# Optimization experiments

Hardware: AMD Instinct MI355X
Metric: run time of the kernel (lower is better)

Reference implementation:

```python
import jax, jax.numpy as jnp
import numpy as np

N_NODES = 100000
N_EDGES = 1600000
D_IN = 128
HID = 128
N_CLS = 10
N_GRAPHS = 128


def _gcn_conv(x, W, b, src, dst, dis, n):
    # x' = W x; out[i] = sum_{(j->i)} d_j^{-1/2} d_i^{-1/2} x'_j ; then + bias
    h = x @ W  # [N, out]
    norm = dis[src] * dis[dst]  # [E_tot]
    msg = h[src] * norm[:, None]  # gather + scale (irregular access)
    out = jax.ops.segment_sum(msg, dst, num_segments=n)  # scatter-add
    return out + b


def setup_inputs() -> dict:
    key = jax.random.key(0)
    ks = jax.random.split(key, 12)
    x = jax.random.normal(ks[0], (N_NODES, D_IN), dtype=jnp.float32)
    edge_index = jax.random.randint(ks[1], (2, N_EDGES), 0, N_NODES, dtype=jnp.int64)
    batch = jnp.sort(jax.random.randint(ks[2], (N_NODES,), 0, N_GRAPHS, dtype=jnp.int64))
    drop_u = jax.random.uniform(ks[3], (N_NODES, D_IN), dtype=jnp.float32)
    s = lambda k, sh, fan: jax.random.normal(k, sh, dtype=jnp.float32) / np.sqrt(fan)
    return {
        "x": x, "edge_index": edge_index, "batch": batch, "num_graphs": N_GRAPHS,
        "drop_u": drop_u,
        "lin1_w": s(ks[4], (D_IN, D_IN), D_IN), "lin1_b": jnp.zeros((D_IN,), jnp.float32),
        "conv1_w": s(ks[5], (D_IN, HID), D_IN), "conv1_b": jnp.zeros((HID,), jnp.float32),
        "conv2_w": s(ks[6], (HID, HID // 2), HID), "conv2_b": jnp.zeros((HID // 2,), jnp.float32),
        "lin2_w": s(ks[7], (HID // 2, N_CLS), HID // 2), "lin2_b": jnp.zeros((N_CLS,), jnp.float32),
    }


def reference(x, edge_index, batch, num_graphs, drop_u,
              lin1_w, lin1_b, conv1_w, conv1_b, conv2_w, conv2_b, lin2_w, lin2_b):
    n = x.shape[0]
    # add self loops (PyG GCNConv default)
    loop = jnp.arange(n, dtype=edge_index.dtype)
    src = jnp.concatenate([edge_index[0], loop])
    dst = jnp.concatenate([edge_index[1], loop])
    deg = jax.ops.segment_sum(jnp.ones_like(dst, dtype=x.dtype), dst, num_segments=n)
    dis = jnp.where(deg > 0, jax.lax.rsqrt(deg), 0.0)  # deg^{-1/2}

    h = x @ lin1_w + lin1_b
    h = _gcn_conv(h, conv1_w, conv1_b, src, dst, dis, n)
    # dropout p=0.5 (training mode in original): keep where u >= 0.5, scale by 2
    h = h * (drop_u >= 0.5).astype(h.dtype) * 2.0
    h = jax.nn.relu(h)
    h = _gcn_conv(h, conv2_w, conv2_b, src, dst, dis, n)
    # global mean pool over graph ids
    sums = jax.ops.segment_sum(h, batch, num_segments=num_graphs)
    cnts = jax.ops.segment_sum(jnp.ones((n,), h.dtype), batch, num_segments=num_graphs)
    pooled = sums / jnp.maximum(cnts, 1.0)[:, None]
    return pooled @ lin2_w + lin2_b
```

## Files before the change

kernel.cpp:

```cpp
#include <hip/hip_runtime.h>
#include <hip/hip_bf16.h>

#define DIN   128
#define HID2  64
#define NCLS  10
#define NGRAPH 128
#define SCAN_CHUNK 1024
#define NBLK 256
#define NBKT_MAX 512
#define CAP 6144

typedef __attribute__((ext_vector_type(8))) short bf16x8;
typedef __attribute__((ext_vector_type(4))) float f32x4;

__device__ __forceinline__ void atomAddF(float* p, float v) {
    unsafeAtomicAdd(p, v);
}

__device__ __forceinline__ unsigned short f2bf(float f) {
    unsigned int u = __float_as_uint(f);
    u += 0x7fffu + ((u >> 16) & 1u);
    return (unsigned short)(u >> 16);
}

__global__ __launch_bounds__(128) void k_w12(const float* __restrict__ lw,
                                             const float* __restrict__ lb,
                                             const float* __restrict__ cw,
                                             const float* __restrict__ cw2,
                                             float* __restrict__ W12,
                                             float* __restrict__ c1preb,
                                             unsigned short* __restrict__ w2b) {
    int i = blockIdx.x, j = threadIdx.x;
    if (i == 129) {
        for (int f = j; f < 8192; f += 128) w2b[f] = f2bf(cw2[f]);
        return;
    }
    const float* arow = (i < 128) ? (lw + i * 128) : lb;
    float acc = 0.f;
#pragma unroll 8
    for (int k = 0; k < 128; ++k) acc += arow[k] * cw[k * 128 + j];
    if (i < 128) W12[i * 128 + j] = acc;
    else         c1preb[j] = acc;
}

__global__ __launch_bounds__(256) void k_bhist(const int* __restrict__ dst,
                                               int* __restrict__ bh, int E, int nbkt,
                                               float* __restrict__ zbuf, int zn) {
    __shared__ int lh[NBKT_MAX];
    if (blockIdx.x == 0)
        for (int i = threadIdx.x; i < zn; i += 256) zbuf[i] = 0.f;
    for (int i = threadIdx.x; i < nbkt; i += 256) lh[i] = 0;
    __syncthreads();
    for (int e = blockIdx.x * 256 + threadIdx.x; e < E; e += NBLK * 256)
        atomicAdd(&lh[__builtin_nontemporal_load(dst + e) >> 8], 1);
    __syncthreads();
    for (int i = threadIdx.x; i < nbkt; i += 256) bh[i * NBLK + blockIdx.x] = lh[i];
}

__global__ __launch_bounds__(256) void k_scan_part(const int* __restrict__ cnt,
                                                   int* __restrict__ part, int n) {
    int base = blockIdx.x * SCAN_CHUNK + threadIdx.x * 4;
    int s = 0;
#pragma unroll
    for (int j = 0; j < 4; ++j) { int i = base + j; if (i < n) s += cnt[i]; }
#pragma unroll
    for (int o = 32; o > 0; o >>= 1) s += __shfl_down(s, o);
    __shared__ int wsum[4];
    if ((threadIdx.x & 63) == 0) wsum[threadIdx.x >> 6] = s;
    __syncthreads();
    if (threadIdx.x == 0) part[blockIdx.x] = wsum[0] + wsum[1] + wsum[2] + wsum[3];
}
__global__ __launch_bounds__(256) void k_scan_mid(int* __restrict__ part,
                                                  int* __restrict__ total_out,
                                                  int B, int n) {
    __shared__ int sh[256];
    int t = threadIdx.x;
    int v = (t < B) ? part[t] : 0;
    sh[t] = v;
    __syncthreads();
    for (int off = 1; off < 256; off <<= 1) {
        int u = (t >= off) ? sh[t - off] : 0;
        __syncthreads();
        sh[t] += u;
        __syncthreads();
    }
    if (t < B) part[t] = sh[t] - v;
    if (t == 255) total_out[n] = sh[255];
}
__global__ __launch_bounds__(256) void k_scan_fin2(const int* cnt,
                                                   const int* __restrict__ part,
                                                   int* out, int n) {
    __shared__ int sh[256];
    int t = threadIdx.x;
    int base = blockIdx.x * SCAN_CHUNK + t * 4;
    int c[4]; int s = 0;
#pragma unroll
    for (int j = 0; j < 4; ++j) { int i = base + j; c[j] = (i < n) ? cnt[i] : 0; s += c[j]; }
    sh[t] = s;
    __syncthreads();
    for (int off = 1; off < 256; off <<= 1) {
        int u = (t >= off) ? sh[t - off] : 0;
        __syncthreads();
        sh[t] += u;
        __syncthreads();
    }
    int excl = part[blockIdx.x] + sh[t] - s;
#pragma unroll
    for (int j = 0; j < 4; ++j) {
        int i = base + j;
        if (i < n) out[i] = excl;
        excl += c[j];
    }
}

__global__ __launch_bounds__(256) void k_partition(const int* __restrict__ src,
                                                   const int* __restrict__ dst,
                                                   const int* __restrict__ bh,
                                                   int* __restrict__ pairs, int E, int nbkt) {
    __shared__ int cur[NBKT_MAX];
    for (int i = threadIdx.x; i < nbkt; i += 256) cur[i] = bh[i * NBLK + blockIdx.x];
    __syncthreads();
    for (int e = blockIdx.x * 256 + threadIdx.x; e < E; e += NBLK * 256) {
        int d = __builtin_nontemporal_load(dst + e);
        int s = __builtin_nontemporal_load(src + e);
        int pos = atomicAdd(&cur[d >> 8], 1);
        pairs[pos] = (s << 8) | (d & 255);
    }
}

__global__ __launch_bounds__(256) void k_csr_local(const int* __restrict__ pairs,
                                                   const int* __restrict__ bh,
                                                   int* __restrict__ row_start,
                                                   float* __restrict__ dis,
                                                   int* __restrict__ col,
                                                   int N) {
    __shared__ int cntL[256], scanL[256], curL[256];
    __shared__ int srcbuf[CAP];
    const int tid = threadIdx.x;
    const int lo = blockIdx.x << 8;
    const int bstart = bh[blockIdx.x * NBLK];
    const int bend = bh[(blockIdx.x + 1) * NBLK];
    const int nE = bend - bstart;

    cntL[tid] = 0;
    __syncthreads();
    for (int e = bstart + tid; e < bend; e += 256)
        atomicAdd(&cntL[pairs[e] & 255], 1);
    __syncthreads();
    const int deg = cntL[tid];
    scanL[tid] = deg;
    __syncthreads();
    for (int off = 1; off < 256; off <<= 1) {
        int u = (tid >= off) ? scanL[tid - off] : 0;
        __syncthreads();
        scanL[tid] += u;
        __syncthreads();
    }
    const int excl = scanL[tid] - deg;
    curL[tid] = excl;
    const int node = lo + tid;
    if (node < N) {
        row_start[node] = bstart + excl;
        dis[node] = rsqrtf((float)(deg + 1));
    } else if (node == N) {
        row_start[N] = bend;
    }
    __syncthreads();
    if (nE <= CAP) {
        for (int e = bstart + tid; e < bend; e += 256) {
            int p = pairs[e];
            int pos = atomicAdd(&curL[p & 255], 1);
            srcbuf[pos] = ((unsigned int)p) >> 8;
        }
        __syncthreads();
        for (int i = tid; i < nE; i += 256)
            col[bstart + i] = srcbuf[i];
    } else {
        for (int e = bstart + tid; e < bend; e += 256) {
            int p = pairs[e];
            int pos = atomicAdd(&curL[p & 255], 1);
            col[bstart + pos] = ((unsigned int)p) >> 8;
        }
    }
}

template <int NCOL>
__global__ __launch_bounds__(256) void k_gemm_mfma(const float* __restrict__ A,
                                                   const float* __restrict__ W,
                                                   const float* __restrict__ bias,
                                                   unsigned short* __restrict__ out, int M) {
    constexpr int KP = 136;
    __shared__ unsigned short As[64 * KP];
    __shared__ unsigned short Wt[NCOL * KP];

    const int tid = threadIdx.x;
    const int row0 = blockIdx.x * 64;

    for (int f = tid; f < 2048; f += 256) {
        int r = f >> 5, c4 = f & 31;
        int gr = row0 + r;
        float4 v = make_float4(0.f, 0.f, 0.f, 0.f);
        if (gr < M) v = *(const float4*)(A + (size_t)gr * 128 + c4 * 4);
        ushort4 b;
        b.x = f2bf(v.x); b.y = f2bf(v.y); b.z = f2bf(v.z); b.w = f2bf(v.w);
        *(ushort4*)(&As[r * KP + c4 * 4]) = b;
    }
    for (int f = tid; f < 32 * NCOL; f += 256) {
        int k = f / (NCOL / 4), n4 = f % (NCOL / 4);
        float4 v = *(const float4*)(W + (size_t)k * NCOL + n4 * 4);
        Wt[(n4 * 4 + 0) * KP + k] = f2bf(v.x);
        Wt[(n4 * 4 + 1) * KP + k] = f2bf(v.y);
        Wt[(n4 * 4 + 2) * KP + k] = f2bf(v.z);
        Wt[(n4 * 4 + 3) * KP + k] = f2bf(v.w);
    }
    __syncthreads();

    const int wave = tid >> 6, lane = tid & 63;
    const int quad = lane >> 4, l16 = lane & 15;
    constexpr int CT = (NCOL == 128) ? 2 : 1;
    const int col0 = wave * 16 * CT;

    f32x4 acc[4][CT];
#pragma unroll
    for (int rt = 0; rt < 4; ++rt)
#pragma unroll
        for (int ct = 0; ct < CT; ++ct) acc[rt][ct] = 0.f;

#pragma unroll
    for (int ks = 0; ks < 4; ++ks) {
        const int kbase = ks * 32 + quad * 8;
        bf16x8 bfr[CT];
#pragma unroll
        for (int ct = 0; ct < CT; ++ct)
            bfr[ct] = *(const bf16x8*)(&Wt[(col0 + ct * 16 + l16) * KP + kbase]);
#pragma unroll
        for (int rt = 0; rt < 4; ++rt) {
            bf16x8 afr = *(const bf16x8*)(&As[(rt * 16 + l16) * KP + kbase]);
#pragma unroll
            for (int ct = 0; ct < CT; ++ct)
                acc[rt][ct] = __builtin_amdgcn_mfma_f32_16x16x32_bf16(afr, bfr[ct], acc[rt][ct], 0, 0, 0);
        }
    }

#pragma unroll
    for (int rt = 0; rt < 4; ++rt)
#pragma unroll
        for (int ct = 0; ct < CT; ++ct) {
            const int c = col0 + ct * 16 + l16;
            const float bv = bias ? bias[c] : 0.f;
#pragma unroll
            for (int reg = 0; reg < 4; ++reg) {
                const int gr = row0 + rt * 16 + quad * 4 + reg;
                if (gr < M) out[(size_t)gr * NCOL + c] = f2bf(acc[rt][ct][reg] + bv);
            }
        }
}

__device__ __forceinline__ void bfacc(uint4 v, float d, float* acc) {
    acc[0] = fmaf(d, __uint_as_float(v.x << 16),        acc[0]);
    acc[1] = fmaf(d, __uint_as_float(v.x & 0xffff0000u), acc[1]);
    acc[2] = fmaf(d, __uint_as_float(v.y << 16),        acc[2]);
    acc[3] = fmaf(d, __uint_as_float(v.y & 0xffff0000u), acc[3]);
    acc[4] = fmaf(d, __uint_as_float(v.z << 16),        acc[4]);
    acc[5] = fmaf(d, __uint_as_float(v.z & 0xffff0000u), acc[5]);
    acc[6] = fmaf(d, __uint_as_float(v.w << 16),        acc[6]);
    acc[7] = fmaf(d, __uint_as_float(v.w & 0xffff0000u), acc[7]);
}

__global__ __launch_bounds__(256) void k_gather_gemm2(const unsigned short* __restrict__ h,
                                                      const int* __restrict__ row_start,
                                                      const int* __restrict__ col,
                                                      const float* __restrict__ dis,
                                                      const float* __restrict__ bias,
                                                      const float* __restrict__ du,
                                                      const unsigned short* __restrict__ w2b,
                                                      unsigned short* __restrict__ h2b,
                                                      int n) {
    constexpr int KP = 136;
    __shared__ unsigned short As[16 * KP];
    __shared__ unsigned short Wt[64 * KP];
    const int tid = threadIdx.x;
    const int node0 = blockIdx.x * 16;
    const int node = node0 + (tid >> 4);
    const int l = tid & 15;
    const int coff = l * 8;

    for (int f = tid; f < 8192; f += 256) {
        int k = f >> 6, c = f & 63;
        Wt[c * KP + k] = w2b[f];
    }

    float r[8];
    if (node < n) {
        const float dn = dis[node];
        float acc[8];
        {
            uint4 v = *(const uint4*)(h + (size_t)node * 128 + coff);
#pragma unroll
            for (int q = 0; q < 8; ++q) acc[q] = 0.f;
            bfacc(v, dn, acc);
        }
        const int beg = row_start[node], end = row_start[node + 1];
        int j = beg;
        for (; j + 3 < end; j += 4) {
            const int s0 = col[j], s1 = col[j + 1], s2 = col[j + 2], s3 = col[j + 3];
            const float d0 = dis[s0], d1 = dis[s1], d2 = dis[s2], d3 = dis[s3];
            const uint4 v0 = *(const uint4*)(h + (size_t)s0 * 128 + coff);
            const uint4 v1 = *(const uint4*)(h + (size_t)s1 * 128 + coff);
            const uint4 v2 = *(const uint4*)(h + (size_t)s2 * 128 + coff);
            const uint4 v3 = *(const uint4*)(h + (size_t)s3 * 128 + coff);
            bfacc(v0, d0, acc);
            bfacc(v1, d1, acc);
            bfacc(v2, d2, acc);
            bfacc(v3, d3, acc);
        }
        for (; j < end; ++j) {
            const int s0 = col[j];
            const float d0 = dis[s0];
            const uint4 v0 = *(const uint4*)(h + (size_t)s0 * 128 + coff);
            bfacc(v0, d0, acc);
        }
        const float4 b0 = *(const float4*)(bias + coff);
        const float4 b1 = *(const float4*)(bias + coff + 4);
        r[0] = fmaf(dn, acc[0], b0.x); r[1] = fmaf(dn, acc[1], b0.y);
        r[2] = fmaf(dn, acc[2], b0.z); r[3] = fmaf(dn, acc[3], b0.w);
        r[4] = fmaf(dn, acc[4], b1.x); r[5] = fmaf(dn, acc[5], b1.y);
        r[6] = fmaf(dn, acc[6], b1.z); r[7] = fmaf(dn, acc[7], b1.w);
        const float4 u0 = *(const float4*)(du + (size_t)node * 128 + coff);
        const float4 u1 = *(const float4*)(du + (size_t)node * 128 + coff + 4);
        r[0] = (u0.x >= 0.5f) ? 2.f * fmaxf(r[0], 0.f) : 0.f;
        r[1] = (u0.y >= 0.5f) ? 2.f * fmaxf(r[1], 0.f) : 0.f;
        r[2] = (u0.z >= 0.5f) ? 2.f * fmaxf(r[2], 0.f) : 0.f;
        r[3] = (u0.w >= 0.5f) ? 2.f * fmaxf(r[3], 0.f) : 0.f;
        r[4] = (u1.x >= 0.5f) ? 2.f * fmaxf(r[4], 0.f) : 0.f;
        r[5] = (u1.y >= 0.5f) ? 2.f * fmaxf(r[5], 0.f) : 0.f;
        r[6] = (u1.z >= 0.5f) ? 2.f * fmaxf(r[6], 0.f) : 0.f;
        r[7] = (u1.w >= 0.5f) ? 2.f * fmaxf(r[7], 0.f) : 0.f;
    } else {
#pragma unroll
        for (int q = 0; q < 8; ++q) r[q] = 0.f;
    }
    ushort4 o0, o1;
    o0.x = f2bf(r[0]); o0.y = f2bf(r[1]); o0.z = f2bf(r[2]); o0.w = f2bf(r[3]);
    o1.x = f2bf(r[4]); o1.y = f2bf(r[5]); o1.z = f2bf(r[6]); o1.w = f2bf(r[7]);
    *(ushort4*)(&As[(tid >> 4) * KP + coff]) = o0;
    *(ushort4*)(&As[(tid >> 4) * KP + coff + 4]) = o1;
    __syncthreads();

    const int wave = tid >> 6, lane = tid & 63;
    const int quad = lane >> 4, l16 = lane & 15;
    const int c0 = wave * 16;
    f32x4 a2 = 0.f;
#pragma unroll
    for (int ks = 0; ks < 4; ++ks) {
        const int kbase = ks * 32 + quad * 8;
        bf16x8 afr = *(const bf16x8*)(&As[l16 * KP + kbase]);
        bf16x8 bfr = *(const bf16x8*)(&Wt[(c0 + l16) * KP + kbase]);
        a2 = __builtin_amdgcn_mfma_f32_16x16x32_bf16(afr, bfr, a2, 0, 0, 0);
    }
#pragma unroll
    for (int reg = 0; reg < 4; ++reg) {
        const int gr = node0 + quad * 4 + reg;
        if (gr < n) h2b[(size_t)gr * 64 + c0 + l16] = f2bf(a2[reg]);
    }
}

__global__ __launch_bounds__(256) void k_gather_pool(const unsigned short* __restrict__ h,
                                                     const int* __restrict__ row_start,
                                                     const int* __restrict__ col,
                                                     const float* __restrict__ dis,
                                                     const float* __restrict__ bias,
                                                     const int* __restrict__ batch,
                                                     float* __restrict__ partial,
                                                     int* __restrict__ bgid,
                                                     int* __restrict__ bvcnt,
                                                     float* __restrict__ sums,
                                                     float* __restrict__ cnt, int n) {
    __shared__ float bsum[4][64];
    __shared__ int sh_gfirst, sh_uni;
    const int tid = threadIdx.x;
    const int node = (blockIdx.x * 256 + tid) >> 3;
    const int l = tid & 7;
    const int coff = l * 8;
    const bool valid = node < n;
    const int node0 = blockIdx.x * 32;

    if (tid == 0) { sh_gfirst = batch[node0]; sh_uni = 1; }
    __syncthreads();
    const int gfirst = sh_gfirst;

    float r[8];
    int g = gfirst;
    if (valid) {
        const float dn = dis[node];
        g = batch[node];
        float acc[8];
        {
            uint4 v = *(const uint4*)(h + (size_t)node * 64 + coff);
#pragma unroll
            for (int q = 0; q < 8; ++q) acc[q] = 0.f;
            bfacc(v, dn, acc);
        }
        const int beg = row_start[node], end = row_start[node + 1];
        int j = beg;
        for (; j + 3 < end; j += 4) {
            const int s0 = col[j], s1 = col[j + 1], s2 = col[j + 2], s3 = col[j + 3];
            const float d0 = dis[s0], d1 = dis[s1], d2 = dis[s2], d3 = dis[s3];
            const uint4 v0 = *(const uint4*)(h + (size_t)s0 * 64 + coff);
            const uint4 v1 = *(const uint4*)(h + (size_t)s1 * 64 + coff);
            const uint4 v2 = *(const uint4*)(h + (size_t)s2 * 64 + coff);
            const uint4 v3 = *(const uint4*)(h + (size_t)s3 * 64 + coff);
            bfacc(v0, d0, acc);
            bfacc(v1, d1, acc);
            bfacc(v2, d2, acc);
            bfacc(v3, d3, acc);
        }
        for (; j < end; ++j) {
            const int s0 = col[j];
            const float d0 = dis[s0];
            const uint4 v0 = *(const uint4*)(h + (size_t)s0 * 64 + coff);
            bfacc(v0, d0, acc);
        }
        const float4 b0 = *(const float4*)(bias + coff);
        const float4 b1 = *(const float4*)(bias + coff + 4);
        r[0] = fmaf(dn, acc[0], b0.x); r[1] = fmaf(dn, acc[1], b0.y);
        r[2] = fmaf(dn, acc[2], b0.z); r[3] = fmaf(dn, acc[3], b0.w);
        r[4] = fmaf(dn, acc[4], b1.x); r[5] = fmaf(dn, acc[5], b1.y);
        r[6] = fmaf(dn, acc[6], b1.z); r[7] = fmaf(dn, acc[7], b1.w);
    } else {
#pragma unroll
        for (int q = 0; q < 8; ++q) r[q] = 0.f;
    }

    if (valid && g != gfirst) atomicAnd(&sh_uni, 0);
    __syncthreads();

    if (sh_uni) {
#pragma unroll
        for (int q = 0; q < 8; ++q) {
            r[q] += __shfl_xor(r[q], 8);
            r[q] += __shfl_xor(r[q], 16);
            r[q] += __shfl_xor(r[q], 32);
        }
        const int wave = tid >> 6, lane = tid & 63;
        if (lane < 8) {
#pragma unroll
            for (int q = 0; q < 8; ++q) bsum[wave][lane * 8 + q] = r[q];
        }
        __syncthreads();
        if (tid < 64)
            partial[(size_t)blockIdx.x * 64 + tid] =
                bsum[0][tid] + bsum[1][tid] + bsum[2][tid] + bsum[3][tid];
        if (tid == 0) {
            bgid[blockIdx.x] = gfirst;
            bvcnt[blockIdx.x] = min(n - node0, 32);
        }
    } else {
        if (tid == 0) bgid[blockIdx.x] = -1;
        const int g0 = __shfl(g, 0);
        const bool wuni = __all(valid && (g == g0));
        if (wuni) {
#pragma unroll
            for (int q = 0; q < 8; ++q) {
                r[q] += __shfl_xor(r[q], 8);
                r[q] += __shfl_xor(r[q], 16);
                r[q] += __shfl_xor(r[q], 32);
            }
            const int lane = tid & 63;
            if (lane < 8) {
#pragma unroll
                for (int q = 0; q < 8; ++q) atomAddF(&sums[g0 * 64 + lane * 8 + q], r[q]);
                if (lane == 0) atomAddF(&cnt[g0], 8.0f);
            }
        } else if (valid) {
#pragma unroll
            for (int q = 0; q < 8; ++q) atomAddF(&sums[g * 64 + coff + q], r[q]);
            if (l == 0) atomAddF(&cnt[g], 1.0f);
        }
    }
}

__global__ __launch_bounds__(256) void k_pool2(const float* __restrict__ partial,
                                               const int* __restrict__ bgid,
                                               const int* __restrict__ bvcnt,
                                               float* __restrict__ sums,
                                               float* __restrict__ cnt, int nb) {
    const int grp = (blockIdx.x * 256 + (int)threadIdx.x) >> 6;
    const int f = threadIdx.x & 63;
    const int ngroups = gridDim.x * 4;
    const int per = (nb + ngroups - 1) / ngroups;
    const int start = grp * per, end = min(nb, start + per);
    if (start >= end) return;
    int cg = -1;
    float acc = 0.f;
    int vc = 0;
    for (int b = start; b < end; ++b) {
        const int g = bgid[b];
        if (g != cg) {
            if (cg >= 0) {
                atomAddF(&sums[cg * 64 + f], acc);
                if (f == 0) atomAddF(&cnt[cg], (float)vc);
            }
            acc = 0.f; vc = 0; cg = g;
        }
        if (g >= 0) {
            acc += partial[(size_t)b * 64 + f];
            vc += bvcnt[b];
        }
    }
    if (cg >= 0) {
        atomAddF(&sums[cg * 64 + f], acc);
        if (f == 0) atomAddF(&cnt[cg], (float)vc);
    }
}

__global__ __launch_bounds__(64) void k_final(const float* __restrict__ sums,
                                              const float* __restrict__ cnt,
                                              const float* __restrict__ w,
                                              const float* __restrict__ b,
                                              float* __restrict__ out) {
    int g = blockIdx.x, f = threadIdx.x;
    float c = fmaxf(cnt[g], 1.0f);
    float p = sums[g * 64 + f] / c;
#pragma unroll
    for (int cls = 0; cls < NCLS; ++cls) {
        float v = p * w[f * 10 + cls];
#pragma unroll
        for (int o = 32; o > 0; o >>= 1) v += __shfl_down(v, o);
        if (f == 0) out[g * 10 + cls] = v + b[cls];
    }
}

extern "C" void kernel_launch(void* const* d_in, const int* in_sizes, int n_in,
                              void* d_out, int out_size, void* d_ws, size_t ws_size,
                              hipStream_t stream) {
    const float* x       = (const float*)d_in[0];
    const int*   ei      = (const int*)d_in[1];
    const int*   batch   = (const int*)d_in[2];
    const float* drop_u  = (const float*)d_in[4];
    const float* lin1_w  = (const float*)d_in[5];
    const float* lin1_b  = (const float*)d_in[6];
    const float* conv1_w = (const float*)d_in[7];
    const float* conv1_b = (const float*)d_in[8];
    const float* conv2_w = (const float*)d_in[9];
    const float* conv2_b = (const float*)d_in[10];
    const float* lin2_w  = (const float*)d_in[11];
    const float* lin2_b  = (const float*)d_in[12];
    float* out = (float*)d_out;

    const int N = in_sizes[0] / DIN;
    const int E = in_sizes[1] / 2;
    const int* src = ei;
    const int* dst = ei + E;

    const int nbkt = (N + 255) >> 8;
    const int M = nbkt * NBLK;
    const int nbGP = (int)(((size_t)N * 8 + 255) / 256);

    float* ws    = (float*)d_ws;
    float* out1  = ws;
    unsigned short* h1b = (unsigned short*)(ws + (size_t)N * 128);
    float* dis   = ws + (size_t)N * 128 + (size_t)N * 64;
    float* W12   = dis + N;
    float* c1pb  = W12 + 16384;
    float* sums  = c1pb + 128;
    float* cntp  = sums + NGRAPH * 64;
    int*   row_start = (int*)(cntp + NGRAPH);
    int*   part  = row_start + N + 2;
    int*   bh    = part + 256;
    int*   col   = bh + NBKT_MAX * NBLK + 2;
    int*   pairs = col + E;
    float* partial = (float*)(pairs + E);
    int*   bgid  = (int*)(partial + (size_t)nbGP * 64);
    int*   bvcnt = bgid + nbGP;
    unsigned short* h2b = (unsigned short*)out1;
    unsigned short* w2b = (unsigned short*)(out1 + (size_t)N * 64);

    k_w12<<<130, 128, 0, stream>>>(lin1_w, lin1_b, conv1_w, conv2_w, W12, c1pb, w2b);

    k_bhist<<<NBLK, 256, 0, stream>>>(dst, bh, E, nbkt, sums, NGRAPH * 64 + NGRAPH);
    const int scanB = (M + SCAN_CHUNK - 1) / SCAN_CHUNK;
    k_scan_part<<<scanB, 256, 0, stream>>>(bh, part, M);
    k_scan_mid<<<1, 256, 0, stream>>>(part, bh, scanB, M);
    k_scan_fin2<<<scanB, 256, 0, stream>>>(bh, part, bh, M);
    k_partition<<<NBLK, 256, 0, stream>>>(src, dst, bh, pairs, E, nbkt);
    k_csr_local<<<nbkt, 256, 0, stream>>>(pairs, bh, row_start, dis, col, N);

    const int gemmGrid = (N + 63) / 64;
    k_gemm_mfma<128><<<gemmGrid, 256, 0, stream>>>(x, W12, c1pb, h1b, N);

    k_gather_gemm2<<<(N + 15) / 16, 256, 0, stream>>>(h1b, row_start, col, dis, conv1_b,
                                                      drop_u, w2b, h2b, N);

    k_gather_pool<<<nbGP, 256, 0, stream>>>(h2b, row_start, col, dis, conv2_b, batch,
                                            partial, bgid, bvcnt, sums, cntp, N);
    k_pool2<<<16, 256, 0, stream>>>(partial, bgid, bvcnt, sums, cntp, nbGP);

    k_final<<<NGRAPH, 64, 0, stream>>>(sums, cntp, lin2_w, lin2_b, out);
}
```

Measured before the change: 379.6 us.

## Precompute dropout bitmask and pre-transpose conv2 weights for vectorized LDS fill

```diff
diff --git a/kernel.cpp b/kernel.cpp
--- a/kernel.cpp
+++ b/kernel.cpp
@@ -32,7 +32,7 @@
                                              unsigned short* __restrict__ w2b) {
     int i = blockIdx.x, j = threadIdx.x;
     if (i == 129) {
-        for (int f = j; f < 8192; f += 128) w2b[f] = f2bf(cw2[f]);
+        for (int f = j; f < 8192; f += 128) w2b[f] = f2bf(cw2[(f & 127) * 64 + (f >> 7)]);
         return;
     }
     const float* arow = (i < 128) ? (lw + i * 128) : lb;
@@ -184,6 +184,23 @@
     }
 }
 
+__global__ __launch_bounds__(256) void k_mask(const float* __restrict__ du,
+                                              unsigned int* __restrict__ dmask, int nw) {
+    const int w = blockIdx.x * 256 + threadIdx.x;
+    if (w >= nw) return;
+    const float* p = du + (size_t)w * 32;
+    unsigned int m = 0;
+#pragma unroll
+    for (int j = 0; j < 8; ++j) {
+        const float4 v = *(const float4*)(p + j * 4);
+        m |= (v.x >= 0.5f ? 1u : 0u) << (j * 4 + 0);
+        m |= (v.y >= 0.5f ? 1u : 0u) << (j * 4 + 1);
+        m |= (v.z >= 0.5f ? 1u : 0u) << (j * 4 + 2);
+        m |= (v.w >= 0.5f ? 1u : 0u) << (j * 4 + 3);
+    }
+    dmask[w] = m;
+}
+
 template <int NCOL>
 __global__ __launch_bounds__(256) void k_gemm_mfma(const float* __restrict__ A,
                                                    const float* __restrict__ W,
@@ -272,7 +289,7 @@
                                                       const int* __restrict__ col,
                                                       const float* __restrict__ dis,
                                                       const float* __restrict__ bias,
-                                                      const float* __restrict__ du,
+                                                      const unsigned int* __restrict__ dmask,
                                                       const unsigned short* __restrict__ w2b,
                                                       unsigned short* __restrict__ h2b,
                                                       int n) {
@@ -285,14 +302,16 @@
     const int l = tid & 15;
     const int coff = l * 8;
 
-    for (int f = tid; f < 8192; f += 256) {
-        int k = f >> 6, c = f & 63;
-        Wt[c * KP + k] = w2b[f];
+    for (int f = tid * 4; f < 8192; f += 1024) {
+        const int c = f >> 7, k = f & 127;
+        *(ushort4*)(&Wt[c * KP + k]) = *(const ushort4*)(&w2b[f]);
     }
 
     float r[8];
     if (node < n) {
         const float dn = dis[node];
+        const unsigned int mword = dmask[node * 4 + (l >> 2)];
+        const unsigned int mbyte = (mword >> ((l & 3) * 8)) & 0xffu;
         float acc[8];
         {
             uint4 v = *(const uint4*)(h + (size_t)node * 128 + coff);
@@ -326,16 +345,9 @@
         r[2] = fmaf(dn, acc[2], b0.z); r[3] = fmaf(dn, acc[3], b0.w);
         r[4] = fmaf(dn, acc[4], b1.x); r[5] = fmaf(dn, acc[5], b1.y);
         r[6] = fmaf(dn, acc[6], b1.z); r[7] = fmaf(dn, acc[7], b1.w);
-        const float4 u0 = *(const float4*)(du + (size_t)node * 128 + coff);
-        const float4 u1 = *(const float4*)(du + (size_t)node * 128 + coff + 4);
-        r[0] = (u0.x >= 0.5f) ? 2.f * fmaxf(r[0], 0.f) : 0.f;
-        r[1] = (u0.y >= 0.5f) ? 2.f * fmaxf(r[1], 0.f) : 0.f;
-        r[2] = (u0.z >= 0.5f) ? 2.f * fmaxf(r[2], 0.f) : 0.f;
-        r[3] = (u0.w >= 0.5f) ? 2.f * fmaxf(r[3], 0.f) : 0.f;
-        r[4] = (u1.x >= 0.5f) ? 2.f * fmaxf(r[4], 0.f) : 0.f;
-        r[5] = (u1.y >= 0.5f) ? 2.f * fmaxf(r[5], 0.f) : 0.f;
-        r[6] = (u1.z >= 0.5f) ? 2.f * fmaxf(r[6], 0.f) : 0.f;
-        r[7] = (u1.w >= 0.5f) ? 2.f * fmaxf(r[7], 0.f) : 0.f;
+#pragma unroll
+        for (int q = 0; q < 8; ++q)
+            r[q] = ((mbyte >> q) & 1u) ? 2.f * fmaxf(r[q], 0.f) : 0.f;
     } else {
 #pragma unroll
         for (int q = 0; q < 8; ++q) r[q] = 0.f;
@@ -573,6 +585,7 @@
     float* partial = (float*)(pairs + E);
     int*   bgid  = (int*)(partial + (size_t)nbGP * 64);
     int*   bvcnt = bgid + nbGP;
+    unsigned int* dmask = (unsigned int*)pairs;
     unsigned short* h2b = (unsigned short*)out1;
     unsigned short* w2b = (unsigned short*)(out1 + (size_t)N * 64);
 
@@ -586,11 +599,13 @@
     k_partition<<<NBLK, 256, 0, stream>>>(src, dst, bh, pairs, E, nbkt);
     k_csr_local<<<nbkt, 256, 0, stream>>>(pairs, bh, row_start, dis, col, N);
 
+    k_mask<<<(N * 4 + 255) / 256, 256, 0, stream>>>(drop_u, dmask, N * 4);
+
     const int gemmGrid = (N + 63) / 64;
     k_gemm_mfma<128><<<gemmGrid, 256, 0, stream>>>(x, W12, c1pb, h1b, N);
 
     k_gather_gemm2<<<(N + 15) / 16, 256, 0, stream>>>(h1b, row_start, col, dis, conv1_b,
-                                                      drop_u, w2b, h2b, N);
+                                                      dmask, w2b, h2b, N);
 
     k_gather_pool<<<nbGP, 256, 0, stream>>>(h2b, row_start, col, dis, conv2_b, batch,
                                             partial, bgid, bvcnt, sums, cntp, N);
```

Measured after the change: 379.3 us. Within noise of the previous version (-0.1%).
